# Optimization experiments

Hardware: AMD Instinct MI355X
Metric: run time of the kernel (lower is better)

The kernel has to match this reference:

```python
import jax, jax.numpy as jnp
import numpy as np

B, FR, D = 32, 300, 2048
E, G, K = 2, 8, 64
FEAT = E * D // G          # 512
VLAD = K * FEAT            # 32768
H, R = 2048, 8
NC = 3862
BN_EPS = 1e-5
L2_EPS = 1e-12


def _bn(x, g, b, m, v):
    # eval-mode BatchNorm1d with running stats
    return (x - m) * jax.lax.rsqrt(v + BN_EPS) * g + b


def _l2n(x, axis):
    # torch F.normalize: x / max(||x||, eps)
    n = jnp.sqrt(jnp.sum(x * x, axis=axis, keepdims=True))
    return x / jnp.maximum(n, L2_EPS)


def setup_inputs() -> dict:
    key = jax.random.key(0)
    ks = jax.random.split(key, 10)
    rn = lambda k, s: jax.random.normal(k, s, jnp.float32) * 0.02
    return {
        "x": jax.random.normal(ks[0], (B, FR, D), jnp.float32),
        "fc1_w": rn(ks[1], (E * D, D)), "fc1_b": jnp.zeros((E * D,), jnp.float32),
        "fc2_w": rn(ks[2], (G, E * D)), "fc2_b": jnp.zeros((G,), jnp.float32),
        "c1": jax.random.uniform(ks[3], (E * D, G * K), jnp.float32),
        "c2": jax.random.uniform(ks[4], (1, FEAT, K), jnp.float32),
        "bn1_g": jnp.ones((G * K,), jnp.float32), "bn1_b": jnp.zeros((G * K,), jnp.float32),
        "bn1_m": jnp.zeros((G * K,), jnp.float32), "bn1_v": jnp.ones((G * K,), jnp.float32),
        "bn2_g": jnp.ones((VLAD,), jnp.float32), "bn2_b": jnp.zeros((VLAD,), jnp.float32),
        "bn2_m": jnp.zeros((VLAD,), jnp.float32), "bn2_v": jnp.ones((VLAD,), jnp.float32),
        "cgf_w": rn(ks[5], (H, VLAD)), "cgf_b": jnp.zeros((H,), jnp.float32),
        "cgbn_g": jnp.ones((H,), jnp.float32), "cgbn_b": jnp.zeros((H,), jnp.float32),
        "cgbn_m": jnp.zeros((H,), jnp.float32), "cgbn_v": jnp.ones((H,), jnp.float32),
        "g1_w": rn(ks[6], (H // R, H)), "g1_b": jnp.zeros((H // R,), jnp.float32),
        "gbn_g": jnp.ones((H // R,), jnp.float32), "gbn_b": jnp.zeros((H // R,), jnp.float32),
        "gbn_m": jnp.zeros((H // R,), jnp.float32), "gbn_v": jnp.ones((H // R,), jnp.float32),
        "g2_w": rn(ks[7], (H, H // R)), "g2_b": jnp.zeros((H,), jnp.float32),
        "fc3_w": rn(ks[8], (NC, H)), "fc3_b": jnp.zeros((NC,), jnp.float32),
    }


def _forward(x, fc1_w, fc1_b, fc2_w, fc2_b, c1, c2,
             bn1_g, bn1_b, bn1_m, bn1_v, bn2_g, bn2_b, bn2_m, bn2_v,
             cgf_w, cgf_b, cgbn_g, cgbn_b, cgbn_m, cgbn_v,
             g1_w, g1_b, gbn_g, gbn_b, gbn_m, gbn_v, g2_w, g2_b, fc3_w, fc3_b):
    b, fr, d = x.shape
    xn = _l2n(x, 2)                                      # per-frame L2 normalize
    h = xn @ fc1_w.T + fc1_b                             # [B,FR,E*D]
    att = jax.nn.sigmoid(h @ fc2_w.T + fc2_b)            # [B,FR,G]
    att = att.reshape(b, fr * G, 1)
    act = jnp.einsum('bfd,dc->bfc', h, c1)               # [B,FR,G*K]
    act = _bn(act, bn1_g, bn1_b, bn1_m, bn1_v)
    act = act.reshape(b, fr * G, K)
    act = jax.nn.softmax(act, axis=-1) * att             # soft-assign * attention
    a = act.sum(axis=1, keepdims=True) * c2              # [B,FEAT,K] via broadcast
    res = h.reshape(b, fr * G, FEAT)
    vlad = jnp.einsum('bnk,bnf->bfk', act, res) - a      # [B,FEAT,K]
    vlad = _l2n(vlad, 1).reshape(b, VLAD)                # intra-norm, flatten feat-major
    vlad = _bn(vlad, bn2_g, bn2_b, bn2_m, bn2_v)
    # SE context gating (dropout identity in reference)
    y = _bn(vlad @ cgf_w.T + cgf_b, cgbn_g, cgbn_b, cgbn_m, cgbn_v)   # [B,H]
    gate = jax.nn.sigmoid(
        jax.nn.relu(_bn(y @ g1_w.T + g1_b, gbn_g, gbn_b, gbn_m, gbn_v)) @ g2_w.T + g2_b)
    return (y * gate) @ fc3_w.T + fc3_b                  # [B,NC]


def reference(x, fc1_w, fc1_b, fc2_w, fc2_b, c1, c2,
              bn1_g, bn1_b, bn1_m, bn1_v, bn2_g, bn2_b, bn2_m, bn2_v,
              cgf_w, cgf_b, cgbn_g, cgbn_b, cgbn_m, cgbn_v,
              g1_w, g1_b, gbn_g, gbn_b, gbn_m, gbn_v, g2_w, g2_b, fc3_w, fc3_b):
    return _forward(x, fc1_w, fc1_b, fc2_w, fc2_b, c1, c2,
                    bn1_g, bn1_b, bn1_m, bn1_v, bn2_g, bn2_b, bn2_m, bn2_v,
                    cgf_w, cgf_b, cgbn_g, cgbn_b, cgbn_m, cgbn_v,
                    g1_w, g1_b, gbn_g, gbn_b, gbn_m, gbn_v, g2_w, g2_b, fc3_w, fc3_b)
```

## Files before the change

### kernel.cpp

```cpp
#include <hip/hip_runtime.h>

typedef unsigned short u16;
typedef unsigned int u32;
using f32x4 = __attribute__((ext_vector_type(4))) float;
using s16x8 = __attribute__((ext_vector_type(8))) short;
using u16x4 = __attribute__((ext_vector_type(4))) u16;

#define DEV __device__ __forceinline__

DEV float bf2f(u16 u) { union { u32 i; float f; } v; v.i = ((u32)u) << 16; return v.f; }
DEV u16 f2bf(float f) {
  union { float ff; u32 uu; } v; v.ff = f;
  u32 r = (v.uu + 0x7fffu + ((v.uu >> 16) & 1u)) >> 16;
  return (u16)r;
}

DEV void gl_lds16(const void* g, void* l) {
  __builtin_amdgcn_global_load_lds(
      (const __attribute__((address_space(1))) u32*)g,
      (__attribute__((address_space(3))) u32*)l, 16, 0, 0);
}

DEV void BAR() { __builtin_amdgcn_s_barrier(); }
DEV void LGKM0() { asm volatile("s_waitcnt lgkmcnt(0)" ::: "memory"); __builtin_amdgcn_sched_barrier(0); }
DEV void VM6() { asm volatile("s_waitcnt vmcnt(6)" ::: "memory"); }
DEV void VM0() { asm volatile("s_waitcnt vmcnt(0)" ::: "memory"); }
DEV void PRIO1() { __builtin_amdgcn_s_setprio(1); }
DEV void PRIO0() { __builtin_amdgcn_s_setprio(0); }

__global__ __launch_bounds__(256) void k_l2norm(const float* __restrict__ x, u16* __restrict__ xn) {
  int r = blockIdx.x, t = threadIdx.x;
  const float* xr = x + (size_t)r * 2048;
  float v[8], s = 0.f;
#pragma unroll
  for (int i = 0; i < 8; i++) { v[i] = xr[t + i*256]; s += v[i]*v[i]; }
#pragma unroll
  for (int off = 32; off > 0; off >>= 1) s += __shfl_xor(s, off, 64);
  __shared__ float red[4];
  if ((t & 63) == 0) red[t >> 6] = s;
  __syncthreads();
  float inv = 1.f / fmaxf(sqrtf(red[0]+red[1]+red[2]+red[3]), 1e-12f);
  u16* xo = xn + (size_t)r * 2048;
#pragma unroll
  for (int i = 0; i < 8; i++) xo[t + i*256] = f2bf(v[i]*inv);
}

__global__ void k_cvt(const float* __restrict__ in, u16* __restrict__ out, int n4) {
  int i = blockIdx.x*256 + threadIdx.x, st = gridDim.x*256;
  for (; i < n4; i += st) {
    f32x4 v = ((const f32x4*)in)[i];
    u16x4 o;
    o[0] = f2bf(v[0]); o[1] = f2bf(v[1]); o[2] = f2bf(v[2]); o[3] = f2bf(v[3]);
    ((u16x4*)out)[i] = o;
  }
}

__global__ __launch_bounds__(256) void k_transpose(const float* __restrict__ c1, u16* __restrict__ c1t) {
  __shared__ float tile[32][33];
  int k0 = blockIdx.x*32, n0 = blockIdx.y*32;
  int tx = threadIdx.x & 31, ty = threadIdx.x >> 5;
  for (int i = ty; i < 32; i += 8) tile[i][tx] = c1[(size_t)(k0+i)*512 + n0 + tx];
  __syncthreads();
  for (int i = ty; i < 32; i += 8) c1t[(size_t)(n0+i)*4096 + k0 + tx] = f2bf(tile[tx][i]);
}

template<bool WF32, bool WBF16>
__global__ __launch_bounds__(256) void k_gemm(
    const u16* __restrict__ A, const u16* __restrict__ Bt, const float* __restrict__ bias,
    float* __restrict__ Cf, u16* __restrict__ Cb, int N, int K, int Nlim,
    int MT, int NT, int swz) {
  __shared__ u16 As[128*32];
  __shared__ u16 Bs[128*32];
  int bid = blockIdx.x, mt, nt;
  if (swz) {
    int mg = (MT + 7) >> 3;
    int gid = bid >> 5, gl = bid & 31;
    mt = (gid % mg)*8 + (gl & 7);
    nt = (gid / mg)*4 + (gl >> 3);
    if (mt >= MT) return;
  } else { mt = bid % MT; nt = bid / MT; }
  int t = threadIdx.x, wv = t >> 6;
  int quad = (t & 63) >> 4, lr = t & 15;
  size_t m0 = (size_t)mt * 128, n0 = (size_t)nt * 128;
  int wm = wv & 1, wn = wv >> 1;
  int srow = t >> 2;
  int scol = (((t & 3) ^ ((t >> 3) & 3)) * 8);
  const u16* gA = A + (m0 + srow)*(size_t)K + scol;
  const u16* gB = Bt + (n0 + srow)*(size_t)K + scol;
  u16* lA = &As[wv*512];
  u16* lB = &Bs[wv*512];
  int xq = (quad ^ ((lr >> 1) & 3)) * 8;
  f32x4 acc[4][4];
#pragma unroll
  for (int i = 0; i < 4; i++)
#pragma unroll
    for (int j = 0; j < 4; j++) acc[i][j] = (f32x4){0.f,0.f,0.f,0.f};
  for (int k0 = 0; k0 < K; k0 += 32) {
    gl_lds16(gA + k0, lA);
    gl_lds16(gA + (size_t)64*K + k0, lA + 2048);
    gl_lds16(gB + k0, lB);
    gl_lds16(gB + (size_t)64*K + k0, lB + 2048);
    __syncthreads();
    s16x8 af[4], bfr[4];
#pragma unroll
    for (int i = 0; i < 4; i++) {
      af[i]  = *(const s16x8*)&As[(wm*64 + i*16 + lr)*32 + xq];
      bfr[i] = *(const s16x8*)&Bs[(wn*64 + i*16 + lr)*32 + xq];
    }
#pragma unroll
    for (int i = 0; i < 4; i++)
#pragma unroll
      for (int j = 0; j < 4; j++)
        acc[i][j] = __builtin_amdgcn_mfma_f32_16x16x32_bf16(af[i], bfr[j], acc[i][j], 0, 0, 0);
    __syncthreads();
  }
#pragma unroll
  for (int j = 0; j < 4; j++) {
    size_t nn = n0 + wn*64 + j*16 + lr;
    if ((int)nn >= Nlim) continue;
    float bj = bias ? bias[nn] : 0.f;
#pragma unroll
    for (int i = 0; i < 4; i++) {
      size_t mr = m0 + wm*64 + i*16 + quad*4;
#pragma unroll
      for (int r = 0; r < 4; r++) {
        float v = acc[i][j][r] + bj;
        if (WF32)  Cf[(mr + r)*N + nn] = v;
        if (WBF16) Cb[(mr + r)*N + nn] = f2bf(v);
      }
    }
  }
}

template<bool WF32, bool WBF16>
__global__ __launch_bounds__(512, 2) void k_gemm256(
    const u16* __restrict__ A, const u16* __restrict__ Bt, const float* __restrict__ bias,
    float* __restrict__ Cf, u16* __restrict__ Cb,
    int M, int N, int K, int Nlim, int MT, int NT, int swz) {
  constexpr int TILE = 256*64;
  __shared__ u16 lds[4*TILE];
  int bid = blockIdx.x;
  if (swz) { int c = (MT*NT) >> 3; bid = (bid & 7)*c + (bid >> 3); }
  int mt = bid % MT, nt = bid / MT;
  int t = threadIdx.x, wv = t >> 6, lane = t & 63;
  int quad = lane >> 4, lr = lane & 15;
  int wm = wv >> 2, wn = wv & 3;
  size_t m0 = (size_t)mt * 256, n0 = (size_t)nt * 256;
  int srow = wv*8 + (lane >> 3);
  int schunk = ((lane & 7) ^ (lane >> 3)) * 8;
  const u16* gA = A  + (size_t)(m0 + srow)*K + schunk;
  const u16* gB = Bt + (size_t)(n0 + srow)*K + schunk;
  size_t row64 = (size_t)64 * K;
  int lofs = wv*512;
  int raBase = (wm*128 + lr)*64;
  int rbBase = (wn*64  + lr)*64;
  int pc0 = ((0 + quad) ^ (lr & 7)) * 8;
  int pc1 = ((4 + quad) ^ (lr & 7)) * 8;
  f32x4 acc[8][4];
#pragma unroll
  for (int i = 0; i < 8; i++)
#pragma unroll
    for (int j = 0; j < 4; j++) acc[i][j] = (f32x4){0.f,0.f,0.f,0.f};

  int T = K >> 6;
  u16* A0 = lds;            u16* B0 = lds + TILE;
  u16* A1 = lds + 2*TILE;   u16* B1 = lds + 3*TILE;
#pragma unroll
  for (int q = 0; q < 4; q++) gl_lds16(gA + q*row64, A0 + q*4096 + lofs);
#pragma unroll
  for (int q = 0; q < 4; q++) gl_lds16(gB + q*row64, B0 + q*4096 + lofs);
#pragma unroll
  for (int q = 0; q < 4; q++) gl_lds16(gA + 64 + q*row64, A1 + q*4096 + lofs);
  gl_lds16(gB + 64 + 0*row64, B1 + 0*4096 + lofs);
  gl_lds16(gB + 64 + 1*row64, B1 + 1*4096 + lofs);
  VM6();
  BAR();

  for (int tt = 0; tt < T; ++tt) {
    u16* Ac = lds + (tt & 1)*(2*TILE);
    u16* Bc = Ac + TILE;
    u16* Bn = lds + ((tt + 1) & 1)*(2*TILE) + TILE;
    s16x8 a[8], b[4];
#pragma unroll
    for (int i = 0; i < 8; i++) a[i] = *(const s16x8*)&Ac[raBase + i*1024 + pc0];
#pragma unroll
    for (int j = 0; j < 4; j++) b[j] = *(const s16x8*)&Bc[rbBase + j*1024 + pc0];
    if (tt + 1 < T) {
      const u16* gB1 = gB + (size_t)(tt + 1)*64;
      gl_lds16(gB1 + 2*row64, Bn + 2*4096 + lofs);
      gl_lds16(gB1 + 3*row64, Bn + 3*4096 + lofs);
    }
    BAR(); LGKM0();
    PRIO1();
#pragma unroll
    for (int i = 0; i < 8; i++) {
      acc[i][0] = __builtin_amdgcn_mfma_f32_16x16x32_bf16(a[i], b[0], acc[i][0], 0, 0, 0);
      acc[i][1] = __builtin_amdgcn_mfma_f32_16x16x32_bf16(a[i], b[1], acc[i][1], 0, 0, 0);
    }
    PRIO0(); BAR();
    PRIO1();
#pragma unroll
    for (int i = 0; i < 8; i++) {
      acc[i][2] = __builtin_amdgcn_mfma_f32_16x16x32_bf16(a[i], b[2], acc[i][2], 0, 0, 0);
      acc[i][3] = __builtin_amdgcn_mfma_f32_16x16x32_bf16(a[i], b[3], acc[i][3], 0, 0, 0);
    }
    PRIO0(); BAR();
#pragma unroll
    for (int i = 0; i < 8; i++) a[i] = *(const s16x8*)&Ac[raBase + i*1024 + pc1];
#pragma unroll
    for (int j = 0; j < 4; j++) b[j] = *(const s16x8*)&Bc[rbBase + j*1024 + pc1];
    BAR(); LGKM0();
    PRIO1();
#pragma unroll
    for (int i = 0; i < 8; i++) {
      acc[i][0] = __builtin_amdgcn_mfma_f32_16x16x32_bf16(a[i], b[0], acc[i][0], 0, 0, 0);
      acc[i][1] = __builtin_amdgcn_mfma_f32_16x16x32_bf16(a[i], b[1], acc[i][1], 0, 0, 0);
    }
    PRIO0(); BAR();
    if (tt + 2 < T) {
      const u16* gA2 = gA + (size_t)(tt + 2)*64;
      const u16* gB2 = gB + (size_t)(tt + 2)*64;
#pragma unroll
      for (int q = 0; q < 4; q++) gl_lds16(gA2 + q*row64, Ac + q*4096 + lofs);
      gl_lds16(gB2 + 0*row64, Bc + 0*4096 + lofs);
      gl_lds16(gB2 + 1*row64, Bc + 1*4096 + lofs);
    }
    BAR();
    PRIO1();
#pragma unroll
    for (int i = 0; i < 8; i++) {
      acc[i][2] = __builtin_amdgcn_mfma_f32_16x16x32_bf16(a[i], b[2], acc[i][2], 0, 0, 0);
      acc[i][3] = __builtin_amdgcn_mfma_f32_16x16x32_bf16(a[i], b[3], acc[i][3], 0, 0, 0);
    }
    PRIO0();
    if (tt + 2 < T) VM6();
    else if (tt + 1 < T) VM0();
    BAR();
  }

#pragma unroll
  for (int j = 0; j < 4; j++) {
    int nn = (int)n0 + wn*64 + j*16 + lr;
    if (nn >= Nlim) continue;
    float bj = bias ? bias[nn] : 0.f;
#pragma unroll
    for (int i = 0; i < 8; i++) {
      int mr = (int)m0 + wm*128 + i*16 + quad*4;
#pragma unroll
      for (int r = 0; r < 4; r++) {
        if (mr + r >= M) continue;
        float v = acc[i][j][r] + bj;
        if (WF32)  Cf[(size_t)(mr + r)*N + nn] = v;
        if (WBF16) Cb[(size_t)(mr + r)*N + nn] = f2bf(v);
      }
    }
  }
}

__global__ __launch_bounds__(256) void k_hbt(const u16* __restrict__ hb, u16* __restrict__ hbT) {
  __shared__ u16 tile[64*33];
  int nt = blockIdx.x, ft = blockIdx.y, b = blockIdx.z, t = threadIdx.x;
  int n0 = nt*32, f0 = ft*64;
  int rrel = t >> 6, g = (t >> 3) & 7, fi = (t & 7)*8;
  const u16* src = hb + ((size_t)(b*300 + (n0 >> 3) + rrel))*4096 + g*512 + f0 + fi;
  u16 v[8];
  *(u16x4*)v = *(const u16x4*)src;
  *(u16x4*)(v+4) = *(const u16x4*)(src+4);
  int nl = rrel*8 + g;
#pragma unroll
  for (int e = 0; e < 8; e++) tile[(fi+e)*33 + nl] = v[e];
  __syncthreads();
  int f = t >> 2, nc = (t & 3)*8;
  u16 o[8];
#pragma unroll
  for (int e = 0; e < 8; e++) o[e] = tile[f*33 + nc + e];
  u16* dst = hbT + ((size_t)b*512 + f0 + f)*2400 + n0 + nc;
  *(u16x4*)dst = *(u16x4*)o;
  *(u16x4*)(dst+4) = *(u16x4*)(o+4);
}

__global__ __launch_bounds__(512) void k_softmax(const float* __restrict__ act_ext,
    const float* __restrict__ fc2_b,
    const float* __restrict__ g, const float* __restrict__ b,
    const float* __restrict__ mu, const float* __restrict__ var, u16* __restrict__ actT) {
  int m = blockIdx.x, t = threadIdx.x;
  int bb = m / 300, fr = m - bb*300;
  int gi = t >> 6, k = t & 63, c = t;
  float v = act_ext[(size_t)m*640 + c];
  v = (v - mu[c]) * rsqrtf(var[c] + 1e-5f) * g[c] + b[c];
  float mx = v;
#pragma unroll
  for (int off = 32; off > 0; off >>= 1) mx = fmaxf(mx, __shfl_xor(mx, off, 64));
  float e = __expf(v - mx);
  float s = e;
#pragma unroll
  for (int off = 32; off > 0; off >>= 1) s += __shfl_xor(s, off, 64);
  float attl = act_ext[(size_t)m*640 + 512 + gi] + fc2_b[gi];
  float attv = 1.f / (1.f + __expf(-attl));
  float r = (e / s) * attv;
  __shared__ u16 st[64*9];
  st[k*9 + gi] = f2bf(r);
  __syncthreads();
  if (t < 64) {
    u16 o[8];
#pragma unroll
    for (int e2 = 0; e2 < 8; e2++) o[e2] = st[t*9 + e2];
    u16* dst = actT + ((size_t)bb*64 + t)*2400 + fr*8;
    *(u16x4*)dst = *(u16x4*)o;
    *(u16x4*)(dst+4) = *(u16x4*)(o+4);
  }
}

__global__ __launch_bounds__(256) void k_asum(const u16* __restrict__ actT, float* __restrict__ a_sum) {
  int b = blockIdx.x, t = threadIdx.x;
  int k = t >> 2, q = t & 3;
  const u16* p = actT + ((size_t)b*64 + k)*2400 + q*600;
  float acc = 0.f;
  for (int j = 0; j < 600; j += 8) {
    u16x4 a0 = *(const u16x4*)(p + j);
    u16x4 a1 = *(const u16x4*)(p + j + 4);
    acc += bf2f(a0[0])+bf2f(a0[1])+bf2f(a0[2])+bf2f(a0[3])
         + bf2f(a1[0])+bf2f(a1[1])+bf2f(a1[2])+bf2f(a1[3]);
  }
  __shared__ float red[256];
  red[t] = acc;
  __syncthreads();
  if (t < 64) a_sum[b*64 + t] = red[t*4] + red[t*4+1] + red[t*4+2] + red[t*4+3];
}

__global__ __launch_bounds__(256) void k_vlad(const u16* __restrict__ hbT, const u16* __restrict__ actT,
                                              float* __restrict__ P2) {
  __shared__ u16 As[128*32];
  __shared__ u16 Bs[64*32];
  int t = threadIdx.x, wv = t >> 6;
  int quad = (t & 63) >> 4, lr = t & 15;
  int ft = blockIdx.x, b = blockIdx.y, ns = blockIdx.z;
  int wm = wv & 1, wn = wv >> 1;
  int srow = t >> 2;
  int scol = (((t & 3) ^ ((t >> 3) & 3)) * 8);
  int xq = (quad ^ ((lr >> 1) & 3)) * 8;
  const u16* gA = hbT + ((size_t)b*512 + ft*128 + srow)*2400 + ns*480 + scol;
  const u16* gB = actT + ((size_t)b*64 + srow)*2400 + ns*480 + scol;
  u16* lA = &As[wv*512];
  u16* lB = &Bs[wv*512];
  f32x4 acc[4][2];
#pragma unroll
  for (int i = 0; i < 4; i++)
#pragma unroll
    for (int j = 0; j < 2; j++) acc[i][j] = (f32x4){0.f,0.f,0.f,0.f};
  for (int k0 = 0; k0 < 480; k0 += 32) {
    gl_lds16(gA + k0, lA);
    gl_lds16(gA + (size_t)64*2400 + k0, lA + 2048);
    gl_lds16(gB + k0, lB);
    __syncthreads();
    s16x8 af[4], bfr[2];
#pragma unroll
    for (int i = 0; i < 4; i++)
      af[i] = *(const s16x8*)&As[(wm*64 + i*16 + lr)*32 + xq];
#pragma unroll
    for (int j = 0; j < 2; j++)
      bfr[j] = *(const s16x8*)&Bs[(wn*32 + j*16 + lr)*32 + xq];
#pragma unroll
    for (int i = 0; i < 4; i++)
#pragma unroll
      for (int j = 0; j < 2; j++)
        acc[i][j] = __builtin_amdgcn_mfma_f32_16x16x32_bf16(af[i], bfr[j], acc[i][j], 0, 0, 0);
    __syncthreads();
  }
  size_t base = ((size_t)ns*32 + b)*512*64;
#pragma unroll
  for (int j = 0; j < 2; j++) {
    int kc = wn*32 + j*16 + lr;
#pragma unroll
    for (int i = 0; i < 4; i++) {
      int f = ft*128 + wm*64 + i*16 + quad*4;
#pragma unroll
      for (int r = 0; r < 4; r++)
        P2[base + (size_t)(f + r)*64 + kc] = acc[i][j][r];
    }
  }
}

__global__ __launch_bounds__(256) void k_norm2(const float* __restrict__ P2, const float* __restrict__ a_sum,
    const float* __restrict__ c2, const float* __restrict__ g, const float* __restrict__ b,
    const float* __restrict__ mu, const float* __restrict__ var, float* __restrict__ out) {
  int k = blockIdx.x, bb = blockIdx.y, t = threadIdx.x;
  float as = a_sum[bb*64 + k];
  int f0 = t, f1 = t + 256;
  const size_t PS = (size_t)32*512*64;
  size_t base = (size_t)bb*512*64;
  float x0 = 0.f, x1 = 0.f;
#pragma unroll
  for (int ns = 0; ns < 5; ns++) {
    x0 += P2[ns*PS + base + (size_t)f0*64 + k];
    x1 += P2[ns*PS + base + (size_t)f1*64 + k];
  }
  x0 -= as * c2[f0*64 + k];
  x1 -= as * c2[f1*64 + k];
  float s = x0*x0 + x1*x1;
#pragma unroll
  for (int off = 32; off > 0; off >>= 1) s += __shfl_xor(s, off, 64);
  __shared__ float red[4];
  if ((t & 63) == 0) red[t >> 6] = s;
  __syncthreads();
  float inv = 1.f / fmaxf(sqrtf(red[0]+red[1]+red[2]+red[3]), 1e-12f);
  int c0 = f0*64 + k, c1 = f1*64 + k;
  out[(size_t)bb*32768 + c0] = (x0*inv - mu[c0]) * rsqrtf(var[c0]+1e-5f) * g[c0] + b[c0];
  out[(size_t)bb*32768 + c1] = (x1*inv - mu[c1]) * rsqrtf(var[c1]+1e-5f) * g[c1] + b[c1];
}

__global__ __launch_bounds__(256) void k_skgemm(
    const float* __restrict__ A, const float* __restrict__ W,
    float* __restrict__ P, int N, int K, int KC, int Npad) {
  constexpr int LDB = 72;
  __shared__ u16 Bs[128*LDB];
  __shared__ u16 As[32*LDB];
  int t = threadIdx.x;
  int wv = t >> 6, quad = (t & 63) >> 4, lr = t & 15;
  int n0 = blockIdx.x * 128;
  size_t kc0 = (size_t)blockIdx.y * KC;
  f32x4 acc[2][2];
#pragma unroll
  for (int i = 0; i < 2; i++)
#pragma unroll
    for (int j = 0; j < 2; j++) acc[i][j] = (f32x4){0.f,0.f,0.f,0.f};
  int wl[8]; size_t wg[8];
#pragma unroll
  for (int i = 0; i < 8; i++) {
    int slot = i*256 + t;
    int r = slot >> 4, q = slot & 15;
    int row = n0 + r; if (row >= N) row = N - 1;
    wl[i] = r*LDB + q*4;
    wg[i] = (size_t)row*K + kc0 + q*4;
  }
  int al[2]; size_t ag[2];
#pragma unroll
  for (int i = 0; i < 2; i++) {
    int slot = i*256 + t;
    int r = slot >> 4, q = slot & 15;
    al[i] = r*LDB + q*4;
    ag[i] = (size_t)r*K + kc0 + q*4;
  }
  int nst = KC >> 6;
  f32x4 wv4[8], av4[2];
#pragma unroll
  for (int i = 0; i < 8; i++) wv4[i] = *(const f32x4*)(W + wg[i]);
#pragma unroll
  for (int i = 0; i < 2; i++) av4[i] = *(const f32x4*)(A + ag[i]);
  for (int s = 0; s < nst; s++) {
    if (s) __syncthreads();
#pragma unroll
    for (int i = 0; i < 8; i++) {
      u16x4 o;
      o[0] = f2bf(wv4[i][0]); o[1] = f2bf(wv4[i][1]);
      o[2] = f2bf(wv4[i][2]); o[3] = f2bf(wv4[i][3]);
      *(u16x4*)&Bs[wl[i]] = o;
    }
#pragma unroll
    for (int i = 0; i < 2; i++) {
      u16x4 o;
      o[0] = f2bf(av4[i][0]); o[1] = f2bf(av4[i][1]);
      o[2] = f2bf(av4[i][2]); o[3] = f2bf(av4[i][3]);
      *(u16x4*)&As[al[i]] = o;
    }
    __syncthreads();
    if (s + 1 < nst) {
      int off = (s + 1) * 64;
#pragma unroll
      for (int i = 0; i < 8; i++) wv4[i] = *(const f32x4*)(W + wg[i] + off);
#pragma unroll
      for (int i = 0; i < 2; i++) av4[i] = *(const f32x4*)(A + ag[i] + off);
    }
#pragma unroll
    for (int ks = 0; ks < 2; ks++) {
      s16x8 af[2];
#pragma unroll
      for (int i = 0; i < 2; i++)
        af[i] = *(const s16x8*)&As[(i*16 + lr)*LDB + ks*32 + quad*8];
#pragma unroll
      for (int j = 0; j < 2; j++) {
        s16x8 bf = *(const s16x8*)&Bs[(wv*32 + j*16 + lr)*LDB + ks*32 + quad*8];
#pragma unroll
        for (int i = 0; i < 2; i++)
          acc[i][j] = __builtin_amdgcn_mfma_f32_16x16x32_bf16(af[i], bf, acc[i][j], 0, 0, 0);
      }
    }
  }
#pragma unroll
  for (int i = 0; i < 2; i++)
#pragma unroll
    for (int j = 0; j < 2; j++) {
      int n = n0 + wv*32 + j*16 + lr;
#pragma unroll
      for (int r = 0; r < 4; r++) {
        int m = i*16 + quad*4 + r;
        P[((size_t)blockIdx.y*32 + m)*Npad + n] = acc[i][j][r];
      }
    }
}

template<int EPI>
__global__ __launch_bounds__(256) void k_skred(const float* __restrict__ P, int KSPLIT, int N, int Npad,
    const float* __restrict__ bias, const float* __restrict__ bg, const float* __restrict__ bb,
    const float* __restrict__ bm, const float* __restrict__ bv, float* __restrict__ C) {
  int idx = blockIdx.x*256 + threadIdx.x;
  if (idx >= 32*N) return;
  int m = idx / N, n = idx - m*N;
  float s = 0.f;
  for (int k = 0; k < KSPLIT; k++) s += P[((size_t)k*32 + m)*Npad + n];
  float v = s + (bias ? bias[n] : 0.f);
  if (EPI == 1 || EPI == 2) {
    v = (v - bm[n]) * rsqrtf(bv[n] + 1e-5f) * bg[n] + bb[n];
    if (EPI == 2) v = fmaxf(v, 0.f);
  } else if (EPI == 3) {
    v = 1.f / (1.f + __expf(-v));
  }
  C[idx] = v;
}

__global__ void k_mul(const float* __restrict__ a, const float* __restrict__ b, float* __restrict__ o, int n) {
  int i = blockIdx.x*256 + threadIdx.x;
  if (i < n) o[i] = a[i]*b[i];
}

extern "C" void kernel_launch(void* const* d_in, const int* in_sizes, int n_in,
                              void* d_out, int out_size, void* d_ws, size_t ws_size,
                              hipStream_t stream) {
  (void)in_sizes; (void)n_in; (void)out_size; (void)ws_size;
  const float* x      = (const float*)d_in[0];
  const float* fc1_w  = (const float*)d_in[1];
  const float* fc1_b  = (const float*)d_in[2];
  const float* fc2_w  = (const float*)d_in[3];
  const float* fc2_b  = (const float*)d_in[4];
  const float* c1     = (const float*)d_in[5];
  const float* c2     = (const float*)d_in[6];
  const float* bn1_g  = (const float*)d_in[7];
  const float* bn1_b  = (const float*)d_in[8];
  const float* bn1_m  = (const float*)d_in[9];
  const float* bn1_v  = (const float*)d_in[10];
  const float* bn2_g  = (const float*)d_in[11];
  const float* bn2_b  = (const float*)d_in[12];
  const float* bn2_m  = (const float*)d_in[13];
  const float* bn2_v  = (const float*)d_in[14];
  const float* cgf_w  = (const float*)d_in[15];
  const float* cgf_b  = (const float*)d_in[16];
  const float* cgbn_g = (const float*)d_in[17];
  const float* cgbn_b = (const float*)d_in[18];
  const float* cgbn_m = (const float*)d_in[19];
  const float* cgbn_v = (const float*)d_in[20];
  const float* g1_w   = (const float*)d_in[21];
  const float* g1_b   = (const float*)d_in[22];
  const float* gbn_g  = (const float*)d_in[23];
  const float* gbn_b  = (const float*)d_in[24];
  const float* gbn_m  = (const float*)d_in[25];
  const float* gbn_v  = (const float*)d_in[26];
  const float* g2_w   = (const float*)d_in[27];
  const float* g2_b   = (const float*)d_in[28];
  const float* fc3_w  = (const float*)d_in[29];
  const float* fc3_b  = (const float*)d_in[30];

  char* w = (char*)d_ws;
  u16*   xn    = (u16*)  (w + 0);
  u16*   w1b   = (u16*)  (w + 39321600);
  u16*   hbT   = (u16*)  (w + 0);
  u16*   hb    = (u16*)  (w + 78643200);
  u16*   c1ext = (u16*)  (w + 157286400);
  float* actx  = (float*)(w + 162529280);
  u16*   actT  = (u16*)  (w + 187105280);
  float* P2    = (float*)(w + 196935680);
  float* P     = (float*)(w + 196935680);
  float* a_sum = (float*)(w + 217907200);
  float* vladn = (float*)(w + 217915392);
  float* y     = (float*)(w + 222109696);
  float* z     = (float*)(w + 222371840);
  float* gate  = (float*)(w + 222404608);
  float* yg    = (float*)(w + 222666752);

  k_l2norm<<<9600, 256, 0, stream>>>(x, xn);
  k_cvt<<<2048, 256, 0, stream>>>(fc1_w, w1b, (4096*2048)/4);
  k_transpose<<<dim3(128, 16), 256, 0, stream>>>(c1, c1ext);
  k_cvt<<<32, 256, 0, stream>>>(fc2_w, c1ext + (size_t)512*4096, (8*4096)/4);
  k_gemm256<false, true><<<608, 512, 0, stream>>>(xn, w1b, fc1_b, nullptr, hb,
                                                  9600, 4096, 2048, 4096, 38, 16, 1);
  k_hbt<<<dim3(75, 8, 32), 256, 0, stream>>>(hb, hbT);
  k_gemm<true, false><<<375, 256, 0, stream>>>(hb, c1ext, nullptr, actx, nullptr, 640, 4096, 520, 75, 5, 0);
  k_softmax<<<9600, 512, 0, stream>>>(actx, fc2_b, bn1_g, bn1_b, bn1_m, bn1_v, actT);
  k_asum<<<32, 256, 0, stream>>>(actT, a_sum);
  k_vlad<<<dim3(4, 32, 5), 256, 0, stream>>>(hbT, actT, P2);
  k_norm2<<<dim3(64, 32), 256, 0, stream>>>(P2, a_sum, c2, bn2_g, bn2_b, bn2_m, bn2_v, vladn);

  k_skgemm<<<dim3(16, 64), 256, 0, stream>>>(vladn, cgf_w, P, 2048, 32768, 512, 2048);
  k_skred<1><<<256, 256, 0, stream>>>(P, 64, 2048, 2048, cgf_b, cgbn_g, cgbn_b, cgbn_m, cgbn_v, y);
  k_skgemm<<<dim3(2, 32), 256, 0, stream>>>(y, g1_w, P, 256, 2048, 64, 256);
  k_skred<2><<<32, 256, 0, stream>>>(P, 32, 256, 256, g1_b, gbn_g, gbn_b, gbn_m, gbn_v, z);
  k_skgemm<<<dim3(16, 4), 256, 0, stream>>>(z, g2_w, P, 2048, 256, 64, 2048);
  k_skred<3><<<256, 256, 0, stream>>>(P, 4, 2048, 2048, g2_b, nullptr, nullptr, nullptr, nullptr, gate);
  k_mul<<<256, 256, 0, stream>>>(y, gate, yg, 65536);
  k_skgemm<<<dim3(31, 16), 256, 0, stream>>>(yg, fc3_w, P, 3862, 2048, 128, 3968);
  k_skred<0><<<483, 256, 0, stream>>>(P, 16, 3862, 3968, fc3_b, nullptr, nullptr, nullptr, nullptr, (float*)d_out);
}
```

Baseline: 1.021 ms.

## Restructure 256-tile GEMM main loop with inline-asm LDS reads and new block swizzle

```diff
diff --git a/kernel.cpp b/kernel.cpp
--- a/kernel.cpp
+++ b/kernel.cpp
@@ -22,11 +22,34 @@
 }
 
 DEV void BAR() { __builtin_amdgcn_s_barrier(); }
-DEV void LGKM0() { asm volatile("s_waitcnt lgkmcnt(0)" ::: "memory"); __builtin_amdgcn_sched_barrier(0); }
 DEV void VM6() { asm volatile("s_waitcnt vmcnt(6)" ::: "memory"); }
 DEV void VM0() { asm volatile("s_waitcnt vmcnt(0)" ::: "memory"); }
 DEV void PRIO1() { __builtin_amdgcn_s_setprio(1); }
 DEV void PRIO0() { __builtin_amdgcn_s_setprio(0); }
+#define LGKM0S() do { asm volatile("s_waitcnt lgkmcnt(0)" ::: "memory"); \
+                      __builtin_amdgcn_sched_barrier(0); } while (0)
+
+#define DSR(d, a, OFF) asm volatile("ds_read_b128 %0, %1 offset:" #OFF \
+                                    : "=&v"(d) : "v"(a))
+#define READ12(A_, B_, aa, bb) do {                                            \
+  unsigned a_ = (aa), b_ = (bb);                                               \
+  DSR(A_[0], a_, 0);     DSR(A_[1], a_, 2048);                                 \
+  DSR(A_[2], a_, 4096);  DSR(A_[3], a_, 6144);                                 \
+  DSR(A_[4], a_, 8192);  DSR(A_[5], a_, 10240);                                \
+  DSR(A_[6], a_, 12288); DSR(A_[7], a_, 14336);                                \
+  DSR(B_[0], b_, 0);     DSR(B_[1], b_, 2048);                                 \
+  DSR(B_[2], b_, 4096);  DSR(B_[3], b_, 6144);                                 \
+} while (0)
+
+#define MFMA32(A_, B_) do {                                                    \
+  _Pragma("unroll")                                                            \
+  for (int i_ = 0; i_ < 8; i_++) {                                             \
+    acc[i_][0] = __builtin_amdgcn_mfma_f32_16x16x32_bf16(A_[i_], B_[0], acc[i_][0], 0, 0, 0); \
+    acc[i_][1] = __builtin_amdgcn_mfma_f32_16x16x32_bf16(A_[i_], B_[1], acc[i_][1], 0, 0, 0); \
+    acc[i_][2] = __builtin_amdgcn_mfma_f32_16x16x32_bf16(A_[i_], B_[2], acc[i_][2], 0, 0, 0); \
+    acc[i_][3] = __builtin_amdgcn_mfma_f32_16x16x32_bf16(A_[i_], B_[3], acc[i_][3], 0, 0, 0); \
+  }                                                                            \
+} while (0)
 
 __global__ __launch_bounds__(256) void k_l2norm(const float* __restrict__ x, u16* __restrict__ xn) {
   int r = blockIdx.x, t = threadIdx.x;
@@ -139,9 +162,15 @@
     int M, int N, int K, int Nlim, int MT, int NT, int swz) {
   constexpr int TILE = 256*64;
   __shared__ u16 lds[4*TILE];
-  int bid = blockIdx.x;
-  if (swz) { int c = (MT*NT) >> 3; bid = (bid & 7)*c + (bid >> 3); }
-  int mt = bid % MT, nt = bid / MT;
+  int bid = blockIdx.x, mt, nt;
+  if (swz == 2) {
+    int x = bid & 7, w2 = bid >> 3;
+    mt = (x & 1)*19 + w2 % 19;
+    nt = (x >> 1)*4 + w2 / 19;
+  } else if (swz == 1) {
+    int c = (MT*NT) >> 3; int b2 = (bid & 7)*c + (bid >> 3);
+    mt = b2 % MT; nt = b2 / MT;
+  } else { mt = bid % MT; nt = bid / MT; }
   int t = threadIdx.x, wv = t >> 6, lane = t & 63;
   int quad = lane >> 4, lr = lane & 15;
   int wm = wv >> 2, wn = wv & 3;
@@ -152,10 +181,10 @@
   const u16* gB = Bt + (size_t)(n0 + srow)*K + schunk;
   size_t row64 = (size_t)64 * K;
   int lofs = wv*512;
-  int raBase = (wm*128 + lr)*64;
-  int rbBase = (wn*64  + lr)*64;
-  int pc0 = ((0 + quad) ^ (lr & 7)) * 8;
-  int pc1 = ((4 + quad) ^ (lr & 7)) * 8;
+  unsigned ldsB = (unsigned)(size_t)lds;
+  unsigned pc = (unsigned)((quad ^ (lr & 7)) << 4);
+  unsigned aCur = ldsB + (unsigned)((wm*128 + lr)*128) + pc;
+  unsigned bCur = ldsB + 32768u + (unsigned)((wn*64 + lr)*128) + pc;
   f32x4 acc[8][4];
 #pragma unroll
   for (int i = 0; i < 8; i++)
@@ -171,87 +200,64 @@
   for (int q = 0; q < 4; q++) gl_lds16(gB + q*row64, B0 + q*4096 + lofs);
 #pragma unroll
   for (int q = 0; q < 4; q++) gl_lds16(gA + 64 + q*row64, A1 + q*4096 + lofs);
-  gl_lds16(gB + 64 + 0*row64, B1 + 0*4096 + lofs);
-  gl_lds16(gB + 64 + 1*row64, B1 + 1*4096 + lofs);
+  gl_lds16(gB + 64,          B1 + lofs);
+  gl_lds16(gB + 64 + row64,  B1 + 4096 + lofs);
   VM6();
   BAR();
 
+  s16x8 fa[8], fb[4];
   for (int tt = 0; tt < T; ++tt) {
-    u16* Ac = lds + (tt & 1)*(2*TILE);
-    u16* Bc = Ac + TILE;
-    u16* Bn = lds + ((tt + 1) & 1)*(2*TILE) + TILE;
-    s16x8 a[8], b[4];
-#pragma unroll
-    for (int i = 0; i < 8; i++) a[i] = *(const s16x8*)&Ac[raBase + i*1024 + pc0];
-#pragma unroll
-    for (int j = 0; j < 4; j++) b[j] = *(const s16x8*)&Bc[rbBase + j*1024 + pc0];
+    READ12(fa, fb, aCur, bCur);
     if (tt + 1 < T) {
       const u16* gB1 = gB + (size_t)(tt + 1)*64;
-      gl_lds16(gB1 + 2*row64, Bn + 2*4096 + lofs);
-      gl_lds16(gB1 + 3*row64, Bn + 3*4096 + lofs);
-    }
-    BAR(); LGKM0();
-    PRIO1();
-#pragma unroll
-    for (int i = 0; i < 8; i++) {
-      acc[i][0] = __builtin_amdgcn_mfma_f32_16x16x32_bf16(a[i], b[0], acc[i][0], 0, 0, 0);
-      acc[i][1] = __builtin_amdgcn_mfma_f32_16x16x32_bf16(a[i], b[1], acc[i][1], 0, 0, 0);
-    }
-    PRIO0(); BAR();
-    PRIO1();
-#pragma unroll
-    for (int i = 0; i < 8; i++) {
-      acc[i][2] = __builtin_amdgcn_mfma_f32_16x16x32_bf16(a[i], b[2], acc[i][2], 0, 0, 0);
-      acc[i][3] = __builtin_amdgcn_mfma_f32_16x16x32_bf16(a[i], b[3], acc[i][3], 0, 0, 0);
-    }
-    PRIO0(); BAR();
-#pragma unroll
-    for (int i = 0; i < 8; i++) a[i] = *(const s16x8*)&Ac[raBase + i*1024 + pc1];
-#pragma unroll
-    for (int j = 0; j < 4; j++) b[j] = *(const s16x8*)&Bc[rbBase + j*1024 + pc1];
-    BAR(); LGKM0();
-    PRIO1();
-#pragma unroll
-    for (int i = 0; i < 8; i++) {
-      acc[i][0] = __builtin_amdgcn_mfma_f32_16x16x32_bf16(a[i], b[0], acc[i][0], 0, 0, 0);
-      acc[i][1] = __builtin_amdgcn_mfma_f32_16x16x32_bf16(a[i], b[1], acc[i][1], 0, 0, 0);
-    }
-    PRIO0(); BAR();
+      u16* Bq = lds + (((tt + 1) & 1)*2 + 1)*TILE;
+      gl_lds16(gB1 + 2*row64, Bq + 2*4096 + lofs);
+      gl_lds16(gB1 + 3*row64, Bq + 3*4096 + lofs);
+    }
+    LGKM0S();
+    PRIO1(); MFMA32(fa, fb); PRIO0();
+    BAR();
+    READ12(fa, fb, aCur ^ 64u, bCur ^ 64u);
+    LGKM0S();
+    PRIO1(); MFMA32(fa, fb); PRIO0();
+    BAR();
     if (tt + 2 < T) {
       const u16* gA2 = gA + (size_t)(tt + 2)*64;
       const u16* gB2 = gB + (size_t)(tt + 2)*64;
-#pragma unroll
-      for (int q = 0; q < 4; q++) gl_lds16(gA2 + q*row64, Ac + q*4096 + lofs);
-      gl_lds16(gB2 + 0*row64, Bc + 0*4096 + lofs);
-      gl_lds16(gB2 + 1*row64, Bc + 1*4096 + lofs);
-    }
-    BAR();
-    PRIO1();
-#pragma unroll
-    for (int i = 0; i < 8; i++) {
-      acc[i][2] = __builtin_amdgcn_mfma_f32_16x16x32_bf16(a[i], b[2], acc[i][2], 0, 0, 0);
-      acc[i][3] = __builtin_amdgcn_mfma_f32_16x16x32_bf16(a[i], b[3], acc[i][3], 0, 0, 0);
-    }
-    PRIO0();
-    if (tt + 2 < T) VM6();
-    else if (tt + 1 < T) VM0();
-    BAR();
-  }
-
+      u16* Ap = lds + ((tt & 1)*2)*TILE;
+      u16* Bp = Ap + TILE;
+#pragma unroll
+      for (int q = 0; q < 4; q++) gl_lds16(gA2 + q*row64, Ap + q*4096 + lofs);
+      gl_lds16(gB2,         Bp + lofs);
+      gl_lds16(gB2 + row64, Bp + 4096 + lofs);
+      VM6();
+    } else if (tt + 1 < T) {
+      VM0();
+    }
+    if (tt + 1 < T) BAR();
+    aCur ^= 0x10000u; bCur ^= 0x10000u;
+  }
+
+  float bj[4];
 #pragma unroll
   for (int j = 0; j < 4; j++) {
     int nn = (int)n0 + wn*64 + j*16 + lr;
-    if (nn >= Nlim) continue;
-    float bj = bias ? bias[nn] : 0.f;
-#pragma unroll
-    for (int i = 0; i < 8; i++) {
-      int mr = (int)m0 + wm*128 + i*16 + quad*4;
-#pragma unroll
-      for (int r = 0; r < 4; r++) {
-        if (mr + r >= M) continue;
-        float v = acc[i][j][r] + bj;
-        if (WF32)  Cf[(size_t)(mr + r)*N + nn] = v;
-        if (WBF16) Cb[(size_t)(mr + r)*N + nn] = f2bf(v);
+    bj[j] = (bias && nn < Nlim) ? bias[nn] : 0.f;
+  }
+#pragma unroll
+  for (int i = 0; i < 8; i++) {
+    int mrb = (int)m0 + wm*128 + i*16 + quad*4;
+#pragma unroll
+    for (int r = 0; r < 4; r++) {
+      int mr = mrb + r;
+      if (mr >= M) continue;
+#pragma unroll
+      for (int j = 0; j < 4; j++) {
+        int nn = (int)n0 + wn*64 + j*16 + lr;
+        if (nn >= Nlim) continue;
+        float v = acc[i][j][r] + bj[j];
+        if (WF32)  Cf[(size_t)mr*N + nn] = v;
+        if (WBF16) Cb[(size_t)mr*N + nn] = f2bf(v);
       }
     }
   }
@@ -581,7 +587,7 @@
   k_transpose<<<dim3(128, 16), 256, 0, stream>>>(c1, c1ext);
   k_cvt<<<32, 256, 0, stream>>>(fc2_w, c1ext + (size_t)512*4096, (8*4096)/4);
   k_gemm256<false, true><<<608, 512, 0, stream>>>(xn, w1b, fc1_b, nullptr, hb,
-                                                  9600, 4096, 2048, 4096, 38, 16, 1);
+                                                  9600, 4096, 2048, 4096, 38, 16, 2);
   k_hbt<<<dim3(75, 8, 32), 256, 0, stream>>>(hb, hbT);
   k_gemm<true, false><<<375, 256, 0, stream>>>(hb, c1ext, nullptr, actx, nullptr, 640, 4096, 520, 75, 5, 0);
   k_softmax<<<9600, 512, 0, stream>>>(actx, fc2_b, bn1_g, bn1_b, bn1_m, bn1_v, actT);
```

New measurement: 1.003 ms. Within noise of the previous version (-1.7%).
